# Performance work log

Hardware: AMD Instinct MI355X
Metric: run time of the kernel (lower is better)

The kernel has to match this reference:

```python
import jax, jax.numpy as jnp
import numpy as np

EMB, NH, NG, T_MAX = 2048, 16, 4, 2048
HD = EMB // NH          # 128
HPG = NH // NG          # 4
B, T = 2, 2048


def _rope_tables(t):
    inv_freq = 1.0 / (10000.0 ** (jnp.arange(0, HD, 2, dtype=jnp.float32) / HD))
    freqs = jnp.outer(jnp.arange(t, dtype=jnp.float32), inv_freq)  # [t, HD//2]
    return jnp.cos(freqs), jnp.sin(freqs)


def _apply_rope(x, cos, sin):
    # x: [..., t, HD], interleaved pairs (0::2 real, 1::2 imag)
    x1 = x[..., 0::2]
    x2 = x[..., 1::2]
    r1 = x1 * cos - x2 * sin
    r2 = x1 * sin + x2 * cos
    return jnp.stack([r1, r2], axis=-1).reshape(x.shape)


def setup_inputs() -> dict:
    key = jax.random.key(0)
    ks = jax.random.split(key, 5)
    s = 0.02
    return {
        "x": jax.random.normal(ks[0], (B, T, EMB), dtype=jnp.float32),
        "Wq": jax.random.normal(ks[1], (EMB, EMB), dtype=jnp.float32) * s,
        "Wk": jax.random.normal(ks[2], (NG * HD, EMB), dtype=jnp.float32) * s,
        "Wv": jax.random.normal(ks[3], (NG * HD, EMB), dtype=jnp.float32) * s,
        "Wo": jax.random.normal(ks[4], (EMB, EMB), dtype=jnp.float32) * s,
    }


def reference(x, Wq, Wk, Wv, Wo):
    b, t, _ = x.shape
    cos, sin = _rope_tables(t)  # [t, HD//2] each; broadcast over batch/heads

    # projections (torch Linear: x @ W.T)
    q = (x @ Wq.T).reshape(b, t, NH, HD).transpose(0, 2, 1, 3)  # [b, NH, t, HD]
    k = (x @ Wk.T).reshape(b, t, NG, HD).transpose(0, 2, 1, 3)  # [b, NG, t, HD]
    v = (x @ Wv.T).reshape(b, t, NG, HD).transpose(0, 2, 1, 3)  # [b, NG, t, HD]

    q = _apply_rope(q, cos, sin)
    k = _apply_rope(k, cos, sin)

    # grouped attention without materializing expanded K/V
    qg = q.reshape(b, NG, HPG, t, HD)                       # [b, g, h, t, d]
    scale = 1.0 / jnp.sqrt(jnp.asarray(HD, dtype=x.dtype))
    scores = jnp.einsum('bghtd,bgsd->bghts', qg, k) * scale  # [b, g, h, t, s]

    causal = jnp.tril(jnp.ones((t, t), dtype=bool))
    scores = jnp.where(causal, scores, jnp.finfo(scores.dtype).min)
    attn = jax.nn.softmax(scores, axis=-1)

    out = jnp.einsum('bghts,bgsd->bghtd', attn, v)           # [b, g, h, t, d]
    out = out.reshape(b, NH, t, HD).transpose(0, 2, 1, 3).reshape(b, t, EMB)
    return out @ Wo.T
```

## Files before the change

### kernel.cpp

```cpp
#include <hip/hip_runtime.h>
#include <stdint.h>
#include <math.h>

#define EMB 2048
#define NHq 16
#define NGk 4
#define HD 128
#define Bb 2
#define Tt 2048
#define MROWS (Bb*Tt)
#define QKVN 3072
#define NQT 32

typedef __bf16 bf16x8 __attribute__((ext_vector_type(8)));
typedef float f32x4 __attribute__((ext_vector_type(4)));
typedef unsigned short u16;
typedef unsigned int u32;

__device__ __forceinline__ u16 f2bf(float f) {
    unsigned int u = __float_as_uint(f);
    u += 0x7fff + ((u >> 16) & 1);
    return (u16)(u >> 16);
}
__device__ __forceinline__ float bf2f(u16 u) {
    return __uint_as_float(((u32)u) << 16);
}
__device__ __forceinline__ u32 cvt_pk_bf16(float lo, float hi) {
    u32 r;
    asm("v_cvt_pk_bf16_f32 %0, %1, %2" : "=v"(r) : "v"(lo), "v"(hi));
    return r;
}

#define GLOAD_LDS16(g, l) \
    __builtin_amdgcn_global_load_lds((const __attribute__((address_space(1))) void*)(g), \
                                     (__attribute__((address_space(3))) void*)(l), 16, 0, 0)

__global__ void cast_bf16_kernel(const float* __restrict__ src, u16* __restrict__ dst, int n4) {
    int i = blockIdx.x * blockDim.x + threadIdx.x;
    if (i < n4) {
        float4 v = reinterpret_cast<const float4*>(src)[i];
        ushort4 o;
        o.x = f2bf(v.x); o.y = f2bf(v.y); o.z = f2bf(v.z); o.w = f2bf(v.w);
        reinterpret_cast<ushort4*>(dst)[i] = o;
    }
}

__global__ void wcast_kernel(const float* __restrict__ Wq, const float* __restrict__ Wk,
                             const float* __restrict__ Wv, const float* __restrict__ Wo,
                             u16* __restrict__ dst) {
    int i = blockIdx.x * blockDim.x + threadIdx.x;
    const float* src; int local;
    if (i < 1048576)      { src = Wq; local = i; }
    else if (i < 1310720) { src = Wk; local = i - 1048576; }
    else if (i < 1572864) { src = Wv; local = i - 1310720; }
    else                  { src = Wo; local = i - 1572864; }
    float4 v = reinterpret_cast<const float4*>(src)[local];
    ushort4 o;
    o.x = f2bf(v.x); o.y = f2bf(v.y); o.z = f2bf(v.z); o.w = f2bf(v.w);
    reinterpret_cast<ushort4*>(dst)[i] = o;
}

__global__ void rope_tables_kernel(float* __restrict__ ctab, float* __restrict__ stab) {
    int t = blockIdx.x, i = threadIdx.x;
    float inv = powf(10000.f, -2.f * (float)i / (float)HD);
    float ang = (float)t * inv;
    ctab[t * 64 + i] = cosf(ang);
    stab[t * 64 + i] = sinf(ang);
}

__global__ void rope_qk_kernel(const u16* __restrict__ lin, const float* __restrict__ ctab,
                               const float* __restrict__ stab, u16* __restrict__ Qb,
                               u16* __restrict__ Kb, float qscale) {
    int i = threadIdx.x;
    int tt = blockIdx.x * 4 + threadIdx.y;
    int hh = blockIdx.y, b = blockIdx.z;
    int coloff; u16* out; float scale;
    if (hh < NHq) { coloff = hh * HD; scale = qscale;
                    out = Qb + (((size_t)(b * NHq + hh)) * Tt + tt) * HD; }
    else { int g = hh - NHq; coloff = EMB + g * HD; scale = 1.f;
           out = Kb + (((size_t)(b * NGk + g)) * Tt + tt) * HD; }
    u32 pair = *reinterpret_cast<const u32*>(&lin[((size_t)(b * Tt + tt)) * QKVN + coloff + 2 * i]);
    float x1 = bf2f((u16)(pair & 0xffff)), x2 = bf2f((u16)(pair >> 16));
    float c = ctab[tt * 64 + i], s = stab[tt * 64 + i];
    ushort2 o;
    o.x = f2bf((x1 * c - x2 * s) * scale);
    o.y = f2bf((x1 * s + x2 * c) * scale);
    *reinterpret_cast<ushort2*>(&out[2 * i]) = o;
}

__global__ void vtrans_kernel(const u16* __restrict__ lin, u16* __restrict__ vt) {
    int tx = threadIdx.x, dy = threadIdx.y;
    int tt = blockIdx.x * 64 + tx;
    int g = blockIdx.y, b = blockIdx.z;
    int ttp = (tt & ~31) | (((tt & 15) << 1) | ((tt >> 4) & 1));
    const u16* src = &lin[((size_t)(b * Tt + tt)) * QKVN + EMB + NGk * HD + g * HD];
    u16* dst = &vt[(((size_t)(b * NGk + g)) * HD) * Tt + ttp];
    #pragma unroll
    for (int k = 0; k < 16; ++k) {
        int d = dy + k * 8;
        dst[(size_t)d * Tt] = src[d];
    }
}

template<int OUTBF>
__global__ __launch_bounds__(256) void gemm_bt(const u16* __restrict__ A, const u16* __restrict__ W,
                                               void* __restrict__ Cout, int M, int N, int K) {
    __shared__ u16 Atile[128 * 32];
    __shared__ u16 Btile[128 * 32];
    const int brow = blockIdx.x * 128;
    const int bcol = blockIdx.y * 128;
    const int t = threadIdx.x;
    const int w = t >> 6, l = t & 63;
    const int lr = l & 15, lq = l >> 4;
    const int wr = (w >> 1) * 64, wc = (w & 1) * 64;
    f32x4 acc[4][4] = {};
    const int nkt = K >> 5;
    for (int kt = 0; kt < nkt; ++kt) {
        const int k0 = kt * 32;
        #pragma unroll
        for (int i = 0; i < 2; ++i) {
            int f = i * 256 + t;
            int row = f >> 2, cb = (f & 3) * 8;
            GLOAD_LDS16(A + (size_t)(brow + row) * K + k0 + cb, &Atile[(i * 256 + w * 64) * 8]);
            GLOAD_LDS16(W + (size_t)(bcol + row) * K + k0 + cb, &Btile[(i * 256 + w * 64) * 8]);
        }
        __syncthreads();
        bf16x8 a[4], b[4];
        #pragma unroll
        for (int m = 0; m < 4; ++m)
            a[m] = *reinterpret_cast<const bf16x8*>(&Atile[(wr + m * 16 + lr) * 32 + lq * 8]);
        #pragma unroll
        for (int n = 0; n < 4; ++n)
            b[n] = *reinterpret_cast<const bf16x8*>(&Btile[(wc + n * 16 + lr) * 32 + lq * 8]);
        #pragma unroll
        for (int m = 0; m < 4; ++m)
            #pragma unroll
            for (int n = 0; n < 4; ++n)
                acc[m][n] = __builtin_amdgcn_mfma_f32_16x16x32_bf16(a[m], b[n], acc[m][n], 0, 0, 0);
        __syncthreads();
    }
    #pragma unroll
    for (int m = 0; m < 4; ++m)
        #pragma unroll
        for (int n = 0; n < 4; ++n)
            #pragma unroll
            for (int r = 0; r < 4; ++r) {
                size_t idx = (size_t)(brow + wr + m * 16 + lq * 4 + r) * N + bcol + wc + n * 16 + lr;
                if (OUTBF) ((u16*)Cout)[idx] = f2bf(acc[m][n][r]);
                else       ((float*)Cout)[idx] = acc[m][n][r];
            }
}

__global__ __launch_bounds__(512) void flash_attn(const u16* __restrict__ Q, const u16* __restrict__ K,
                                                  const u16* __restrict__ Vt, u16* __restrict__ Out) {
    __shared__ __align__(16) char smem[73728];
    u16* KldsBase = (u16*)smem;
    u16* VldsBase = (u16*)(smem + 32768);
    const int h = blockIdx.y;
    const int b = blockIdx.z;
    const int ilo = (b == 0) ? blockIdx.x : (NQT / 2 - 1 - blockIdx.x);
    const int ihi = NQT - 1 - ilo;
    const int g = h >> 2;
    const int t = threadIdx.x;
    const int w = t >> 6, l = t & 63;
    const int wq = w & 3, half = w >> 2;
    const int lr = l & 15, lq = l >> 4;
    char* Pw = smem + 65536 + w * 1024;

    const size_t qhead = ((size_t)(b * NHq + h)) * Tt;
    const size_t qblo = (qhead + ilo * 64 + wq * 16) * HD;
    const size_t qbhi = (qhead + ihi * 64 + wq * 16) * HD;
    bf16x8 qfl[4], qfh[4];
    #pragma unroll
    for (int d = 0; d < 4; ++d) {
        qfl[d] = *reinterpret_cast<const bf16x8*>(&Q[qblo + (size_t)lr * HD + d * 32 + lq * 8]);
        qfh[d] = *reinterpret_cast<const bf16x8*>(&Q[qbhi + (size_t)lr * HD + d * 32 + lq * 8]);
    }
    bf16x8 ones;
    #pragma unroll
    for (int j = 0; j < 8; ++j) ones[j] = (__bf16)1.0f;

    f32x4 ol[8] = {}, oh[8] = {};
    f32x4 lsl = {}, lsh = {};

    const int qlo0 = ilo * 64 + wq * 16 + lq * 4;
    const int qhi0 = ihi * 64 + wq * 16 + lq * 4;
    const size_t kbase  = ((size_t)(b * NGk + g)) * Tt * HD;
    const size_t vtbase = ((size_t)(b * NGk + g)) * HD * Tt;
    const int nkt = NQT - ilo;

    int kofs[2], vofs[2];
    #pragma unroll
    for (int j = 0; j < 2; ++j) {
        int krow = j * 32 + w * 4 + (l >> 4);
        kofs[j] = krow * HD + (((l & 15) ^ (krow & 7)) * 8);
        int vrow = j * 64 + w * 8 + (l >> 3);
        vofs[j] = vrow * (int)Tt + (((l & 7) ^ (vrow & 7)) * 8);
    }

    #pragma unroll
    for (int j = 0; j < 2; ++j) {
        GLOAD_LDS16(K + kbase + kofs[j], KldsBase + (j * 512 + w * 64) * 8);
        GLOAD_LDS16(Vt + vtbase + vofs[j], VldsBase + (j * 512 + w * 64) * 8);
    }
    int cur = 0;

    for (int kt = 0; kt < nkt; ++kt) {
        const int kp0 = kt * 64;
        __syncthreads();
        if (kt + 1 < nkt) {
            #pragma unroll
            for (int j = 0; j < 2; ++j) {
                GLOAD_LDS16(K + kbase + (size_t)(kp0 + 64) * HD + kofs[j],
                            KldsBase + (cur ^ 1) * 8192 + (j * 512 + w * 64) * 8);
                GLOAD_LDS16(Vt + vtbase + (kp0 + 64) + vofs[j],
                            VldsBase + (cur ^ 1) * 8192 + (j * 512 + w * 64) * 8);
            }
        }
        const char* Kb = smem + cur * 16384;
        const char* Vb = smem + 32768 + cur * 16384;

        const bool lo_act = (kt <= ilo);
        f32x4 sl[2] = {}, sh[2] = {};
        __builtin_amdgcn_s_setprio(1);
        #pragma unroll
        for (int ct = 0; ct < 2; ++ct) {
            #pragma unroll
            for (int d = 0; d < 4; ++d) {
                int row = half * 32 + ct * 16 + lr;
                int bo = row * 256 + ((d * 64 + lq * 16) ^ ((row & 7) << 4));
                bf16x8 kf = *reinterpret_cast<const bf16x8*>(Kb + bo);
                if (lo_act) sl[ct] = __builtin_amdgcn_mfma_f32_16x16x32_bf16(qfl[d], kf, sl[ct], 0, 0, 0);
                sh[ct] = __builtin_amdgcn_mfma_f32_16x16x32_bf16(qfh[d], kf, sh[ct], 0, 0, 0);
            }
        }
        __builtin_amdgcn_s_setprio(0);

        {
            const bool diag = (kt == nkt - 1);
            float e[2][4];
            #pragma unroll
            for (int ct = 0; ct < 2; ++ct)
                #pragma unroll
                for (int r = 0; r < 4; ++r) {
                    float v = sh[ct][r];
                    if (diag && (kp0 + half * 32 + ct * 16 + lr > qhi0 + r)) v = -1e30f;
                    e[ct][r] = exp2f(v);
                }
            #pragma unroll
            for (int r = 0; r < 4; ++r) {
                int row = lq * 4 + r;
                int bo = row * 64 + (((lr >> 2) ^ (row & 3)) << 4) + (lr & 3) * 4;
                *reinterpret_cast<u32*>(Pw + bo) = cvt_pk_bf16(e[0][r], e[1][r]);
            }
        }
        bf16x8 pfh = *reinterpret_cast<const bf16x8*>(Pw + lr * 64 + ((lq ^ (lr & 3)) << 4));
        bf16x8 pfl;
        if (lo_act) {
            const bool diag = (kt == ilo);
            float e[2][4];
            #pragma unroll
            for (int ct = 0; ct < 2; ++ct)
                #pragma unroll
                for (int r = 0; r < 4; ++r) {
                    float v = sl[ct][r];
                    if (diag && (kp0 + half * 32 + ct * 16 + lr > qlo0 + r)) v = -1e30f;
                    e[ct][r] = exp2f(v);
                }
            #pragma unroll
            for (int r = 0; r < 4; ++r) {
                int row = lq * 4 + r;
                int bo = row * 64 + (((lr >> 2) ^ (row & 3)) << 4) + (lr & 3) * 4;
                *reinterpret_cast<u32*>(Pw + bo) = cvt_pk_bf16(e[0][r], e[1][r]);
            }
            pfl = *reinterpret_cast<const bf16x8*>(Pw + lr * 64 + ((lq ^ (lr & 3)) << 4));
        }

        __builtin_amdgcn_s_setprio(1);
        #pragma unroll
        for (int n = 0; n < 8; ++n) {
            int vrow = n * 16 + lr;
            int bv = vrow * 128 + ((half * 64 + lq * 16) ^ ((vrow & 7) << 4));
            bf16x8 vf = *reinterpret_cast<const bf16x8*>(Vb + bv);
            oh[n] = __builtin_amdgcn_mfma_f32_16x16x32_bf16(pfh, vf, oh[n], 0, 0, 0);
            if (lo_act) ol[n] = __builtin_amdgcn_mfma_f32_16x16x32_bf16(pfl, vf, ol[n], 0, 0, 0);
        }
        lsh = __builtin_amdgcn_mfma_f32_16x16x32_bf16(pfh, ones, lsh, 0, 0, 0);
        if (lo_act) lsl = __builtin_amdgcn_mfma_f32_16x16x32_bf16(pfl, ones, lsl, 0, 0, 0);
        __builtin_amdgcn_s_setprio(0);
        cur ^= 1;
    }

    __syncthreads();
    float* Osh = (float*)smem;
    float* Lsh = (float*)(smem + 65536);
    if (half == 1) {
        #pragma unroll
        for (int n = 0; n < 8; ++n)
            #pragma unroll
            for (int r = 0; r < 4; ++r) {
                int row = lq * 4 + r, col = n * 16 + lr;
                Osh[(wq * 32 + row) * 128 + col] = oh[n][r];
                Osh[(wq * 32 + 16 + row) * 128 + col] = ol[n][r];
            }
        if (lr == 0) {
            #pragma unroll
            for (int r = 0; r < 4; ++r) {
                Lsh[wq * 32 + lq * 4 + r] = lsh[r];
                Lsh[wq * 32 + 16 + lq * 4 + r] = lsl[r];
            }
        }
    }
    __syncthreads();
    if (half == 0) {
        float invh[4], invl[4];
        #pragma unroll
        for (int r = 0; r < 4; ++r) {
            invh[r] = 1.f / (lsh[r] + Lsh[wq * 32 + lq * 4 + r]);
            invl[r] = 1.f / (lsl[r] + Lsh[wq * 32 + 16 + lq * 4 + r]);
        }
        const size_t obase = ((size_t)b * Tt) * EMB + (size_t)h * HD;
        #pragma unroll
        for (int n = 0; n < 8; ++n)
            #pragma unroll
            for (int r = 0; r < 4; ++r) {
                int row = lq * 4 + r, col = n * 16 + lr;
                float vh = oh[n][r] + Osh[(wq * 32 + row) * 128 + col];
                float vl = ol[n][r] + Osh[(wq * 32 + 16 + row) * 128 + col];
                int rh = ihi * 64 + wq * 16 + row;
                int rl = ilo * 64 + wq * 16 + row;
                Out[obase + (size_t)rh * EMB + col] = f2bf(vh * invh[r]);
                Out[obase + (size_t)rl * EMB + col] = f2bf(vl * invl[r]);
            }
    }
}

extern "C" void kernel_launch(void* const* d_in, const int* in_sizes, int n_in,
                              void* d_out, int out_size, void* d_ws, size_t ws_size,
                              hipStream_t stream) {
    (void)in_sizes; (void)n_in; (void)out_size; (void)ws_size;
    const float* x  = (const float*)d_in[0];
    const float* Wq = (const float*)d_in[1];
    const float* Wk = (const float*)d_in[2];
    const float* Wv = (const float*)d_in[3];
    const float* Wo = (const float*)d_in[4];
    float* out = (float*)d_out;

    char* ws = (char*)d_ws;
    size_t off = 0;
    auto alloc = [&](size_t bytes) { char* p = ws + off; off += (bytes + 255) & ~(size_t)255; return p; };

    u16* w_bf    = (u16*)alloc((size_t)(QKVN * EMB + EMB * EMB) * 2);
    u16* x_bf    = (u16*)alloc((size_t)MROWS * EMB * 2);
    u16* qkv_lin = (u16*)alloc((size_t)MROWS * QKVN * 4);
    u16* Qb      = (u16*)alloc((size_t)Bb * NHq * Tt * HD * 2);
    u16* Kb      = (u16*)alloc((size_t)Bb * NGk * Tt * HD * 2);
    u16* Vtb     = (u16*)alloc((size_t)Bb * NGk * HD * Tt * 2);
    float* ctab  = (float*)alloc((size_t)Tt * 64 * 4);
    float* stab  = (float*)alloc((size_t)Tt * 64 * 4);
    u16* attnout = qkv_lin;

    u16* wo_bf = w_bf + (size_t)QKVN * EMB;

    cast_bf16_kernel<<<(MROWS * EMB / 4 + 255) / 256, 256, 0, stream>>>(x, x_bf, MROWS * EMB / 4);
    wcast_kernel<<<(QKVN * EMB + EMB * EMB) / 4 / 256, 256, 0, stream>>>(Wq, Wk, Wv, Wo, w_bf);
    rope_tables_kernel<<<Tt, 64, 0, stream>>>(ctab, stab);

    gemm_bt<1><<<dim3(MROWS / 128, QKVN / 128), 256, 0, stream>>>(x_bf, w_bf, qkv_lin, MROWS, QKVN, EMB);

    const float qscale = 1.44269504088896f / sqrtf((float)HD);
    rope_qk_kernel<<<dim3(Tt / 4, NHq + NGk, Bb), dim3(64, 4), 0, stream>>>(qkv_lin, ctab, stab, Qb, Kb, qscale);
    vtrans_kernel<<<dim3(Tt / 64, NGk, Bb), dim3(64, 8), 0, stream>>>(qkv_lin, Vtb);

    flash_attn<<<dim3(NQT / 2, NHq, Bb), 512, 0, stream>>>(Qb, Kb, Vtb, attnout);

    gemm_bt<0><<<dim3(MROWS / 128, EMB / 128), 256, 0, stream>>>(attnout, wo_bf, out, MROWS, EMB, EMB);
}
```

Before: 250.6 us.

## Swap MFMA operand order to keep P in registers and drop LDS round-trip

The attention kernel now computes S^T by swapping the MFMA A/B operands. Each lane's score accumulators then form the bf16x8 P fragment directly in registers, so the per-wave LDS write/read of P is removed. The V-transpose permutation is changed to match the new fragment ordering. The epilogue is rewritten to use vectorized f32x4 LDS stores into a padded buffer and packed bf16 global stores. The causal mask now zeroes exponentials after exp2 instead of biasing the scores. LDS use drops slightly.

```diff
diff --git a/kernel.cpp b/kernel.cpp
--- a/kernel.cpp
+++ b/kernel.cpp
@@ -14,6 +14,7 @@
 
 typedef __bf16 bf16x8 __attribute__((ext_vector_type(8)));
 typedef float f32x4 __attribute__((ext_vector_type(4)));
+typedef unsigned int u32x4 __attribute__((ext_vector_type(4)));
 typedef unsigned short u16;
 typedef unsigned int u32;
 
@@ -92,7 +93,7 @@
     int tx = threadIdx.x, dy = threadIdx.y;
     int tt = blockIdx.x * 64 + tx;
     int g = blockIdx.y, b = blockIdx.z;
-    int ttp = (tt & ~31) | (((tt & 15) << 1) | ((tt >> 4) & 1));
+    int ttp = (tt & ~31) | (((tt >> 2) & 3) * 8 + ((tt >> 4) & 1) * 4 + (tt & 3));
     const u16* src = &lin[((size_t)(b * Tt + tt)) * QKVN + EMB + NGk * HD + g * HD];
     u16* dst = &vt[(((size_t)(b * NGk + g)) * HD) * Tt + ttp];
     #pragma unroll
@@ -153,7 +154,7 @@
 
 __global__ __launch_bounds__(512) void flash_attn(const u16* __restrict__ Q, const u16* __restrict__ K,
                                                   const u16* __restrict__ Vt, u16* __restrict__ Out) {
-    __shared__ __align__(16) char smem[73728];
+    __shared__ __align__(16) char smem[69632];
     u16* KldsBase = (u16*)smem;
     u16* VldsBase = (u16*)(smem + 32768);
     const int h = blockIdx.y;
@@ -165,7 +166,6 @@
     const int w = t >> 6, l = t & 63;
     const int wq = w & 3, half = w >> 2;
     const int lr = l & 15, lq = l >> 4;
-    char* Pw = smem + 65536 + w * 1024;
 
     const size_t qhead = ((size_t)(b * NHq + h)) * Tt;
     const size_t qblo = (qhead + ilo * 64 + wq * 16) * HD;
@@ -183,8 +183,8 @@
     f32x4 ol[8] = {}, oh[8] = {};
     f32x4 lsl = {}, lsh = {};
 
-    const int qlo0 = ilo * 64 + wq * 16 + lq * 4;
-    const int qhi0 = ihi * 64 + wq * 16 + lq * 4;
+    const int qlo = ilo * 64 + wq * 16 + lr;
+    const int qhi = ihi * 64 + wq * 16 + lr;
     const size_t kbase  = ((size_t)(b * NGk + g)) * Tt * HD;
     const size_t vtbase = ((size_t)(b * NGk + g)) * HD * Tt;
     const int nkt = NQT - ilo;
@@ -230,50 +230,57 @@
                 int row = half * 32 + ct * 16 + lr;
                 int bo = row * 256 + ((d * 64 + lq * 16) ^ ((row & 7) << 4));
                 bf16x8 kf = *reinterpret_cast<const bf16x8*>(Kb + bo);
-                if (lo_act) sl[ct] = __builtin_amdgcn_mfma_f32_16x16x32_bf16(qfl[d], kf, sl[ct], 0, 0, 0);
-                sh[ct] = __builtin_amdgcn_mfma_f32_16x16x32_bf16(qfh[d], kf, sh[ct], 0, 0, 0);
+                sh[ct] = __builtin_amdgcn_mfma_f32_16x16x32_bf16(kf, qfh[d], sh[ct], 0, 0, 0);
+                if (lo_act) sl[ct] = __builtin_amdgcn_mfma_f32_16x16x32_bf16(kf, qfl[d], sl[ct], 0, 0, 0);
             }
         }
         __builtin_amdgcn_s_setprio(0);
 
+        const int kvb = kp0 + half * 32 + lq * 4;
+        bf16x8 pfh, pfl;
         {
             const bool diag = (kt == nkt - 1);
             float e[2][4];
             #pragma unroll
             for (int ct = 0; ct < 2; ++ct)
                 #pragma unroll
-                for (int r = 0; r < 4; ++r) {
-                    float v = sh[ct][r];
-                    if (diag && (kp0 + half * 32 + ct * 16 + lr > qhi0 + r)) v = -1e30f;
-                    e[ct][r] = exp2f(v);
-                }
-            #pragma unroll
-            for (int r = 0; r < 4; ++r) {
-                int row = lq * 4 + r;
-                int bo = row * 64 + (((lr >> 2) ^ (row & 3)) << 4) + (lr & 3) * 4;
-                *reinterpret_cast<u32*>(Pw + bo) = cvt_pk_bf16(e[0][r], e[1][r]);
-            }
-        }
-        bf16x8 pfh = *reinterpret_cast<const bf16x8*>(Pw + lr * 64 + ((lq ^ (lr & 3)) << 4));
-        bf16x8 pfl;
+                for (int r = 0; r < 4; ++r)
+                    e[ct][r] = exp2f(sh[ct][r]);
+            if (diag) {
+                #pragma unroll
+                for (int ct = 0; ct < 2; ++ct)
+                    #pragma unroll
+                    for (int r = 0; r < 4; ++r)
+                        if (kvb + ct * 16 + r > qhi) e[ct][r] = 0.f;
+            }
+            u32x4 pk;
+            pk[0] = cvt_pk_bf16(e[0][0], e[0][1]);
+            pk[1] = cvt_pk_bf16(e[0][2], e[0][3]);
+            pk[2] = cvt_pk_bf16(e[1][0], e[1][1]);
+            pk[3] = cvt_pk_bf16(e[1][2], e[1][3]);
+            pfh = __builtin_bit_cast(bf16x8, pk);
+        }
         if (lo_act) {
             const bool diag = (kt == ilo);
             float e[2][4];
             #pragma unroll
             for (int ct = 0; ct < 2; ++ct)
                 #pragma unroll
-                for (int r = 0; r < 4; ++r) {
-                    float v = sl[ct][r];
-                    if (diag && (kp0 + half * 32 + ct * 16 + lr > qlo0 + r)) v = -1e30f;
-                    e[ct][r] = exp2f(v);
-                }
-            #pragma unroll
-            for (int r = 0; r < 4; ++r) {
-                int row = lq * 4 + r;
-                int bo = row * 64 + (((lr >> 2) ^ (row & 3)) << 4) + (lr & 3) * 4;
-                *reinterpret_cast<u32*>(Pw + bo) = cvt_pk_bf16(e[0][r], e[1][r]);
-            }
-            pfl = *reinterpret_cast<const bf16x8*>(Pw + lr * 64 + ((lq ^ (lr & 3)) << 4));
+                for (int r = 0; r < 4; ++r)
+                    e[ct][r] = exp2f(sl[ct][r]);
+            if (diag) {
+                #pragma unroll
+                for (int ct = 0; ct < 2; ++ct)
+                    #pragma unroll
+                    for (int r = 0; r < 4; ++r)
+                        if (kvb + ct * 16 + r > qlo) e[ct][r] = 0.f;
+            }
+            u32x4 pk;
+            pk[0] = cvt_pk_bf16(e[0][0], e[0][1]);
+            pk[1] = cvt_pk_bf16(e[0][2], e[0][3]);
+            pk[2] = cvt_pk_bf16(e[1][0], e[1][1]);
+            pk[3] = cvt_pk_bf16(e[1][2], e[1][3]);
+            pfl = __builtin_bit_cast(bf16x8, pk);
         }
 
         __builtin_amdgcn_s_setprio(1);
@@ -282,56 +289,47 @@
             int vrow = n * 16 + lr;
             int bv = vrow * 128 + ((half * 64 + lq * 16) ^ ((vrow & 7) << 4));
             bf16x8 vf = *reinterpret_cast<const bf16x8*>(Vb + bv);
-            oh[n] = __builtin_amdgcn_mfma_f32_16x16x32_bf16(pfh, vf, oh[n], 0, 0, 0);
-            if (lo_act) ol[n] = __builtin_amdgcn_mfma_f32_16x16x32_bf16(pfl, vf, ol[n], 0, 0, 0);
-        }
-        lsh = __builtin_amdgcn_mfma_f32_16x16x32_bf16(pfh, ones, lsh, 0, 0, 0);
-        if (lo_act) lsl = __builtin_amdgcn_mfma_f32_16x16x32_bf16(pfl, ones, lsl, 0, 0, 0);
+            oh[n] = __builtin_amdgcn_mfma_f32_16x16x32_bf16(vf, pfh, oh[n], 0, 0, 0);
+            if (lo_act) ol[n] = __builtin_amdgcn_mfma_f32_16x16x32_bf16(vf, pfl, ol[n], 0, 0, 0);
+        }
+        lsh = __builtin_amdgcn_mfma_f32_16x16x32_bf16(ones, pfh, lsh, 0, 0, 0);
+        if (lo_act) lsl = __builtin_amdgcn_mfma_f32_16x16x32_bf16(ones, pfl, lsl, 0, 0, 0);
         __builtin_amdgcn_s_setprio(0);
         cur ^= 1;
     }
 
     __syncthreads();
     float* Osh = (float*)smem;
-    float* Lsh = (float*)(smem + 65536);
+    float* Lsh = (float*)(smem + 128 * 132 * 4);
     if (half == 1) {
         #pragma unroll
-        for (int n = 0; n < 8; ++n)
-            #pragma unroll
-            for (int r = 0; r < 4; ++r) {
-                int row = lq * 4 + r, col = n * 16 + lr;
-                Osh[(wq * 32 + row) * 128 + col] = oh[n][r];
-                Osh[(wq * 32 + 16 + row) * 128 + col] = ol[n][r];
-            }
-        if (lr == 0) {
-            #pragma unroll
-            for (int r = 0; r < 4; ++r) {
-                Lsh[wq * 32 + lq * 4 + r] = lsh[r];
-                Lsh[wq * 32 + 16 + lq * 4 + r] = lsl[r];
-            }
+        for (int n = 0; n < 8; ++n) {
+            *reinterpret_cast<f32x4*>(&Osh[(wq * 32 + lr) * 132 + n * 16 + lq * 4]) = oh[n];
+            *reinterpret_cast<f32x4*>(&Osh[(wq * 32 + 16 + lr) * 132 + n * 16 + lq * 4]) = ol[n];
+        }
+        if (lq == 0) {
+            Lsh[wq * 32 + lr] = lsh[0];
+            Lsh[wq * 32 + 16 + lr] = lsl[0];
         }
     }
     __syncthreads();
     if (half == 0) {
-        float invh[4], invl[4];
-        #pragma unroll
-        for (int r = 0; r < 4; ++r) {
-            invh[r] = 1.f / (lsh[r] + Lsh[wq * 32 + lq * 4 + r]);
-            invl[r] = 1.f / (lsl[r] + Lsh[wq * 32 + 16 + lq * 4 + r]);
-        }
-        const size_t obase = ((size_t)b * Tt) * EMB + (size_t)h * HD;
-        #pragma unroll
-        for (int n = 0; n < 8; ++n)
-            #pragma unroll
-            for (int r = 0; r < 4; ++r) {
-                int row = lq * 4 + r, col = n * 16 + lr;
-                float vh = oh[n][r] + Osh[(wq * 32 + row) * 128 + col];
-                float vl = ol[n][r] + Osh[(wq * 32 + 16 + row) * 128 + col];
-                int rh = ihi * 64 + wq * 16 + row;
-                int rl = ilo * 64 + wq * 16 + row;
-                Out[obase + (size_t)rh * EMB + col] = f2bf(vh * invh[r]);
-                Out[obase + (size_t)rl * EMB + col] = f2bf(vl * invl[r]);
-            }
+        const float invh = 1.f / (lsh[0] + Lsh[wq * 32 + lr]);
+        const float invl = 1.f / (lsl[0] + Lsh[wq * 32 + 16 + lr]);
+        u16* outh = Out + ((size_t)(b * Tt) + ihi * 64 + wq * 16 + lr) * EMB + h * HD;
+        u16* outl = Out + ((size_t)(b * Tt) + ilo * 64 + wq * 16 + lr) * EMB + h * HD;
+        #pragma unroll
+        for (int n = 0; n < 8; ++n) {
+            f32x4 sh4 = *reinterpret_cast<const f32x4*>(&Osh[(wq * 32 + lr) * 132 + n * 16 + lq * 4]);
+            f32x4 sl4 = *reinterpret_cast<const f32x4*>(&Osh[(wq * 32 + 16 + lr) * 132 + n * 16 + lq * 4]);
+            uint2 ph, pl;
+            ph.x = cvt_pk_bf16((oh[n][0] + sh4[0]) * invh, (oh[n][1] + sh4[1]) * invh);
+            ph.y = cvt_pk_bf16((oh[n][2] + sh4[2]) * invh, (oh[n][3] + sh4[3]) * invh);
+            pl.x = cvt_pk_bf16((ol[n][0] + sl4[0]) * invl, (ol[n][1] + sl4[1]) * invl);
+            pl.y = cvt_pk_bf16((ol[n][2] + sl4[2]) * invl, (ol[n][3] + sl4[3]) * invl);
+            *reinterpret_cast<uint2*>(&outh[n * 16 + lq * 4]) = ph;
+            *reinterpret_cast<uint2*>(&outl[n * 16 + lq * 4]) = pl;
+        }
     }
 }
 
```

Result: faster. 240.7 us (-4.0%).
